# Optimization experiments

Hardware: AMD Instinct MI355X
Metric: run time of the kernel (lower is better)

The kernel has to match this reference:

```python
import jax, jax.numpy as jnp
import numpy as np

C_S = 128
C_T = 128
C_OUT = 128


def _proj(x, W, b):
    # 1x1x1 Conv3d == per-voxel linear over channel dim. x: [B, Cin, T, H, W]
    return jnp.einsum('oc,bcthw->bothw', W, x) + b[None, :, None, None, None]


def setup_inputs() -> dict:
    key = jax.random.key(0)
    ks = jax.random.split(key, 12)
    B, T, H, W = 4, 4, 32, 32
    spatial_features = jax.random.normal(ks[0], (B, T, C_S, H, W), dtype=jnp.float32)
    temporal_features = jax.random.normal(ks[1], (B, C_T, T, H, W), dtype=jnp.float32)
    def w(k, o, i):
        return jax.random.normal(k, (o, i), dtype=jnp.float32) * (i ** -0.5)
    return {
        'spatial_features': spatial_features,
        'temporal_features': temporal_features,
        'Wq': w(ks[2], C_OUT, C_S), 'bq': jnp.zeros((C_OUT,), jnp.float32),
        'Wk': w(ks[3], C_OUT, C_T), 'bk': jnp.zeros((C_OUT,), jnp.float32),
        'Wv': w(ks[4], C_OUT, C_T), 'bv': jnp.zeros((C_OUT,), jnp.float32),
        'Wo': w(ks[5], C_OUT, C_OUT), 'bo': jnp.zeros((C_OUT,), jnp.float32),
    }


def reference(spatial_features, temporal_features, Wq, bq, Wk, bk, Wv, bv, Wo, bo):
    B, T, C_s, H, W = spatial_features.shape
    N = T * H * W
    scale = C_OUT ** -0.5
    # permute(0,2,1,3,4): [B, T, C_s, H, W] -> [B, C_s, T, H, W]
    x_s = jnp.transpose(spatial_features, (0, 2, 1, 3, 4))
    q = _proj(x_s, Wq, bq)                 # [B, C_out, T, H, W]
    k = _proj(temporal_features, Wk, bk)   # [B, C_out, T, H, W]
    v = _proj(temporal_features, Wv, bv)   # [B, C_out, T, H, W]
    Q = q.reshape(B, C_OUT, N).transpose(0, 2, 1)  # [B, N, C]
    K = k.reshape(B, C_OUT, N)                     # [B, C, N]
    V = v.reshape(B, C_OUT, N).transpose(0, 2, 1)  # [B, N, C]
    attn = jax.nn.softmax(jnp.einsum('bnc,bcm->bnm', Q, K) * scale, axis=2)  # [B, N, N]
    out = jnp.einsum('bnm,bmc->bnc', attn, V)      # [B, N, C]
    out = out.transpose(0, 2, 1).reshape(B, C_OUT, T, H, W)
    return _proj(out, Wo, bo)
```

## Files before the change

kernel.cpp:

```cpp
#include <hip/hip_runtime.h>
#include <cstddef>

#define NDIM 4096
#define SCALE 0.08838834764831843f
#define SOFT_BIAS 8.0f

typedef _Float16 h8 __attribute__((ext_vector_type(8)));
typedef _Float16 h4 __attribute__((ext_vector_type(4)));
typedef _Float16 h2 __attribute__((ext_vector_type(2)));
typedef float    f4 __attribute__((ext_vector_type(4)));

__device__ __forceinline__ h8 cvt_w_frag(const float* wp) {
    const float4 u0 = *(const float4*)wp;
    const float4 u1 = *(const float4*)(wp + 4);
    h8 f;
    f[0]=(_Float16)u0.x; f[1]=(_Float16)u0.y; f[2]=(_Float16)u0.z; f[3]=(_Float16)u0.w;
    f[4]=(_Float16)u1.x; f[5]=(_Float16)u1.y; f[6]=(_Float16)u1.z; f[7]=(_Float16)u1.w;
    return f;
}

__global__ __launch_bounds__(256) void prep_w_kernel(
    const float* __restrict__ Wq, const float* __restrict__ Wk,
    const float* __restrict__ Wv, const float* __restrict__ Wo,
    _Float16* __restrict__ Whf)
{
    const int gid = blockIdx.x * 256 + threadIdx.x;
    const int mat = gid >> 11, rem = gid & 2047;
    const int ot = rem >> 8, ks = (rem >> 6) & 3, l = rem & 63;
    const float* src = mat == 0 ? Wq : mat == 1 ? Wk : mat == 2 ? Wv : Wo;
    const h8 f = cvt_w_frag(src + (size_t)(16 * ot + (l & 15)) * 128 + 32 * ks + 8 * (l >> 4));
    *(h8*)(Whf + (size_t)gid * 8) = f;
}

__global__ __launch_bounds__(256, 3) void proj_qkv_kernel(
    const float* __restrict__ spatial, const float* __restrict__ temporal,
    const _Float16* __restrict__ Whf,
    const float* __restrict__ bq, const float* __restrict__ bk,
    const float* __restrict__ bv,
    _Float16* __restrict__ Qh, _Float16* __restrict__ Kh, _Float16* __restrict__ Vt)
{
    __shared__ __align__(16) _Float16 Xl[32 * 136];
    const int tid = threadIdx.x;
    const int n0  = blockIdx.x * 32;
    const int b   = blockIdx.y;
    const int p   = blockIdx.z;
    const float* __restrict__ bias = (p == 0) ? bq : (p == 1) ? bk : bv;

    {
        const float* src; size_t rs;
        if (p == 0) { const int t = n0 >> 10, hw0 = n0 & 1023;
            src = spatial + (((size_t)(b * 4 + t) * 128) << 10) + hw0; rs = 1024; }
        else { src = temporal + ((size_t)(b * 128) << 12) + n0; rs = 4096; }
        #pragma unroll
        for (int i = 0; i < 2; ++i) {
            const int ii = tid + 256 * i;
            const int c2 = ii >> 3, j = ii & 7;
            const float4 v0 = *(const float4*)(src + (size_t)(2 * c2) * rs + 4 * j);
            const float4 v1 = *(const float4*)(src + (size_t)(2 * c2 + 1) * rs + 4 * j);
            const float a0[4] = {v0.x, v0.y, v0.z, v0.w};
            const float a1[4] = {v1.x, v1.y, v1.z, v1.w};
            #pragma unroll
            for (int u = 0; u < 4; ++u) {
                h2 pk; pk[0] = (_Float16)a0[u]; pk[1] = (_Float16)a1[u];
                *(h2*)&Xl[(4 * j + u) * 136 + 2 * c2] = pk;
            }
        }
    }
    __syncthreads();

    const int w = tid >> 6, lane = tid & 63, n16 = tid & 15, q4 = (tid >> 4) & 3;

    h8 wf[2][4];
    #pragma unroll
    for (int otl = 0; otl < 2; ++otl)
        #pragma unroll
        for (int ks = 0; ks < 4; ++ks)
            wf[otl][ks] = *(const h8*)(Whf + ((size_t)(((p * 8 + 2 * w + otl) * 4 + ks)) << 9)
                                           + lane * 8);
    h8 xf[2][4];
    #pragma unroll
    for (int ns = 0; ns < 2; ++ns)
        #pragma unroll
        for (int ks = 0; ks < 4; ++ks)
            xf[ns][ks] = *(const h8*)&Xl[(16 * ns + n16) * 136 + 32 * ks + 8 * q4];

    if (p < 2) {
        f4 acc[2][2];
        #pragma unroll
        for (int i = 0; i < 2; ++i) { acc[i][0] = (f4)0.0f; acc[i][1] = (f4)0.0f; }
        #pragma unroll
        for (int otl = 0; otl < 2; ++otl)
            #pragma unroll
            for (int ns = 0; ns < 2; ++ns)
                #pragma unroll
                for (int ks = 0; ks < 4; ++ks)
                    acc[otl][ns] = __builtin_amdgcn_mfma_f32_16x16x32_f16(
                        wf[otl][ks], xf[ns][ks], acc[otl][ns], 0, 0, 0);
        _Float16* __restrict__ dst = (p == 0) ? Qh : Kh;
        #pragma unroll
        for (int otl = 0; otl < 2; ++otl) {
            const float4 bb = *(const float4*)&bias[16 * (2 * w + otl) + 4 * q4];
            #pragma unroll
            for (int ns = 0; ns < 2; ++ns) {
                h4 r;
                r[0]=(_Float16)(acc[otl][ns][0]+bb.x); r[1]=(_Float16)(acc[otl][ns][1]+bb.y);
                r[2]=(_Float16)(acc[otl][ns][2]+bb.z); r[3]=(_Float16)(acc[otl][ns][3]+bb.w);
                *(h4*)(dst + ((size_t)b * NDIM + n0 + 16 * ns + n16) * 128
                           + 16 * (2 * w + otl) + 4 * q4) = r;
            }
        }
    } else {
        f4 acc[2][2];
        #pragma unroll
        for (int i = 0; i < 2; ++i) { acc[i][0] = (f4)0.0f; acc[i][1] = (f4)0.0f; }
        #pragma unroll
        for (int ns = 0; ns < 2; ++ns)
            #pragma unroll
            for (int otl = 0; otl < 2; ++otl)
                #pragma unroll
                for (int ks = 0; ks < 4; ++ks)
                    acc[ns][otl] = __builtin_amdgcn_mfma_f32_16x16x32_f16(
                        xf[ns][ks], wf[otl][ks], acc[ns][otl], 0, 0, 0);
        #pragma unroll
        for (int ns = 0; ns < 2; ++ns)
            #pragma unroll
            for (int otl = 0; otl < 2; ++otl) {
                const float bb = bias[16 * (2 * w + otl) + n16];
                h4 r;
                r[0]=(_Float16)(acc[ns][otl][0]+bb); r[1]=(_Float16)(acc[ns][otl][1]+bb);
                r[2]=(_Float16)(acc[ns][otl][2]+bb); r[3]=(_Float16)(acc[ns][otl][3]+bb);
                *(h4*)(Vt + ((size_t)(b * 128 + 16 * (2 * w + otl) + n16) << 12)
                          + n0 + 16 * ns + 4 * q4) = r;
            }
    }
}

__global__ __launch_bounds__(256, 2) void attn_kernel(
    const _Float16* __restrict__ Qh, const _Float16* __restrict__ Kh,
    const _Float16* __restrict__ Vt, _Float16* __restrict__ Opart,
    float* __restrict__ lpart)
{
    __shared__ __align__(16) _Float16 sh[29184];

    const int tid  = threadIdx.x;
    const int w    = tid >> 6, lane = tid & 63;
    const int g    = w >> 1,  p    = w & 1;
    const int n16  = lane & 15, q4 = lane >> 4;
    const int b    = blockIdx.z, hf = blockIdx.y;
    const int n0   = blockIdx.x * 128;
    const int mb   = hf * 1024;

    h8 qf[4][4];
    {
        const _Float16* Qb = Qh + ((size_t)b * NDIM + n0 + 64 * g + n16) * 128;
        #pragma unroll
        for (int qs = 0; qs < 4; ++qs)
            #pragma unroll
            for (int ks = 0; ks < 4; ++ks)
                qf[qs][ks] = *(const h8*)(Qb + (size_t)(16 * qs) * 128 + 32 * ks + 8 * q4);
    }

    const int km  = tid >> 4, kc8 = (tid & 15) * 8;
    const int vc  = tid >> 2, vm8 = (tid & 3) * 8;
    const _Float16* kp = Kh + ((size_t)b * NDIM + mb + km) * 128 + kc8;
    const _Float16* vp = Vt + (((size_t)(b * 128 + vc)) << 12) + mb + vm8;

    int4 kreg0 = *(const int4*)kp;
    int4 kreg1 = *(const int4*)(kp + (size_t)16 * 128);
    int4 vreg0 = *(const int4*)vp;
    int4 vreg1 = *(const int4*)(vp + ((size_t)64 << 12));
    *(int4*)&sh[km * 136 + kc8]        = kreg0;
    *(int4*)&sh[(16 + km) * 136 + kc8] = kreg1;
    kp += 32 * 128;
    kreg0 = *(const int4*)kp;
    kreg1 = *(const int4*)(kp + (size_t)16 * 128);

    f4 oacc[4][4];
    #pragma unroll
    for (int i = 0; i < 4; ++i)
        #pragma unroll
        for (int j = 0; j < 4; ++j) oacc[i][j] = (f4)0.0f;
    float lsum[4] = {0.0f, 0.0f, 0.0f, 0.0f};

    for (int it = 0; it < 32; ++it) {
        __syncthreads();
        const int cur = it & 1, prv = cur ^ 1;
        _Float16* __restrict__ KB = sh + cur * 4352;
        _Float16* __restrict__ KO = sh + prv * 4352;
        _Float16* __restrict__ VB = sh + 8704  + cur * 5120;
        const _Float16* __restrict__ VP = sh + 8704 + prv * 5120;
        _Float16* __restrict__ Pg = sh + 18944 + cur * 5120 + g * 2560;
        const _Float16* __restrict__ Pp = sh + 18944 + prv * 5120 + g * 2560;

        if (it > 0) {
            h8 pf[4], vf[4];
            #pragma unroll
            for (int qs = 0; qs < 4; ++qs)
                pf[qs] = *(const h8*)&Pp[(16 * qs + n16) * 40 + 8 * q4];
            #pragma unroll
            for (int ct = 0; ct < 4; ++ct)
                vf[ct] = *(const h8*)&VP[(64 * p + 16 * ct + n16) * 40 + 8 * q4];
            #pragma unroll
            for (int qs = 0; qs < 4; ++qs)
                #pragma unroll
                for (int ct = 0; ct < 4; ++ct)
                    oacc[qs][ct] = __builtin_amdgcn_mfma_f32_16x16x32_f16(
                        pf[qs], vf[ct], oacc[qs][ct], 0, 0, 0);
        }

        {
            f4 sacc[4];
            #pragma unroll
            for (int qs = 0; qs < 4; ++qs) sacc[qs] = (f4)0.0f;
            #pragma unroll
            for (int ks = 0; ks < 4; ++ks) {
                const h8 kf = *(const h8*)&KB[(16 * p + n16) * 136 + 32 * ks + 8 * q4];
                #pragma unroll
                for (int qs = 0; qs < 4; ++qs)
                    sacc[qs] = __builtin_amdgcn_mfma_f32_16x16x32_f16(kf, qf[qs][ks], sacc[qs], 0, 0, 0);
            }
            #pragma unroll
            for (int qs = 0; qs < 4; ++qs) {
                h4 pk;
                #pragma unroll
                for (int r = 0; r < 4; ++r) {
                    const float e = __expf(fmaf(sacc[qs][r], SCALE, -SOFT_BIAS));
                    lsum[qs] += e;
                    pk[r] = (_Float16)e;
                }
                *(h4*)&Pg[(16 * qs + n16) * 40 + 16 * p + 4 * q4] = pk;
            }
        }

        *(int4*)&VB[vc * 40 + vm8]        = vreg0;
        *(int4*)&VB[(64 + vc) * 40 + vm8] = vreg1;
        if (it < 31) {
            *(int4*)&KO[km * 136 + kc8]        = kreg0;
            *(int4*)&KO[(16 + km) * 136 + kc8] = kreg1;
            vp += 32;
            vreg0 = *(const int4*)vp;
            vreg1 = *(const int4*)(vp + ((size_t)64 << 12));
        }
        if (it < 30) {
            kp += 32 * 128;
            kreg0 = *(const int4*)kp;
            kreg1 = *(const int4*)(kp + (size_t)16 * 128);
        }
    }

    __syncthreads();
    {
        const _Float16* __restrict__ Pp = sh + 18944 + 5120 + g * 2560;
        const _Float16* __restrict__ VP = sh + 8704  + 5120;
        h8 pf[4], vf[4];
        #pragma unroll
        for (int qs = 0; qs < 4; ++qs)
            pf[qs] = *(const h8*)&Pp[(16 * qs + n16) * 40 + 8 * q4];
        #pragma unroll
        for (int ct = 0; ct < 4; ++ct)
            vf[ct] = *(const h8*)&VP[(64 * p + 16 * ct + n16) * 40 + 8 * q4];
        #pragma unroll
        for (int qs = 0; qs < 4; ++qs)
            #pragma unroll
            for (int ct = 0; ct < 4; ++ct)
                oacc[qs][ct] = __builtin_amdgcn_mfma_f32_16x16x32_f16(
                    pf[qs], vf[ct], oacc[qs][ct], 0, 0, 0);
    }

    #pragma unroll
    for (int qs = 0; qs < 4; ++qs) {
        lsum[qs] += __shfl_xor(lsum[qs], 16, 64);
        lsum[qs] += __shfl_xor(lsum[qs], 32, 64);
    }
    if (q4 == 0) {
        float* lb = lpart + ((size_t)((hf * 2 + p) * 4 + b)) * NDIM + n0 + 64 * g;
        #pragma unroll
        for (int qs = 0; qs < 4; ++qs) lb[16 * qs + n16] = lsum[qs];
    }

    __syncthreads();
    #pragma unroll
    for (int qs = 0; qs < 4; ++qs)
        #pragma unroll
        for (int ct = 0; ct < 4; ++ct)
            #pragma unroll
            for (int r = 0; r < 4; ++r)
                sh[(64 * g + 16 * qs + 4 * q4 + r) * 136 + 64 * p + 16 * ct + n16] =
                    (_Float16)oacc[qs][ct][r];
    __syncthreads();
    const size_t ob = ((size_t)(hf * 4 + b) * NDIM + n0) * 128;
    #pragma unroll
    for (int i = 0; i < 8; ++i) {
        const int ii  = tid + 256 * i;
        const int row = ii >> 4, c8 = (ii & 15) * 8;
        *(int4*)(Opart + ob + (size_t)row * 128 + c8) = *(const int4*)&sh[row * 136 + c8];
    }
}

__global__ __launch_bounds__(256, 2) void proj_final_kernel(
    const _Float16* __restrict__ Opart, const float* __restrict__ lpart,
    const _Float16* __restrict__ Whf, const float* __restrict__ bo,
    float* __restrict__ out)
{
    __shared__ __align__(16) _Float16 Xl[32 * 136];
    __shared__ float lrow[32];
    __shared__ __align__(16) float Ofin[128 * 36];
    const int tid = threadIdx.x;
    const int n0  = blockIdx.x * 32;
    const int b   = blockIdx.y;

    if (tid < 32) {
        float l = 0.0f;
        #pragma unroll
        for (int h8i = 0; h8i < 8; ++h8i)
            l += lpart[((size_t)(h8i * 4 + b)) * NDIM + n0 + tid];
        lrow[tid] = 1.0f / l;
    }
    float vals[2][8];
    int rows[2], c8s[2];
    #pragma unroll
    for (int i = 0; i < 2; ++i) {
        const int ii = tid + 256 * i;
        rows[i] = ii >> 4; c8s[i] = (ii & 15) * 8;
        #pragma unroll
        for (int j = 0; j < 8; ++j) vals[i][j] = 0.0f;
        #pragma unroll
        for (int hf = 0; hf < 4; ++hf) {
            const h8 o = *(const h8*)(Opart + ((size_t)(hf * 4 + b) * NDIM + n0 + rows[i]) * 128
                                      + c8s[i]);
            #pragma unroll
            for (int j = 0; j < 8; ++j) vals[i][j] += (float)o[j];
        }
    }
    __syncthreads();
    #pragma unroll
    for (int i = 0; i < 2; ++i) {
        const float linv = lrow[rows[i]];
        h8 r;
        #pragma unroll
        for (int j = 0; j < 8; ++j) r[j] = (_Float16)(vals[i][j] * linv);
        *(h8*)&Xl[rows[i] * 136 + c8s[i]] = r;
    }
    __syncthreads();

    const int w = tid >> 6, lane = tid & 63, n16 = tid & 15, q4 = (tid >> 4) & 3;

    h8 wf[2][4];
    #pragma unroll
    for (int otl = 0; otl < 2; ++otl)
        #pragma unroll
        for (int ks = 0; ks < 4; ++ks)
            wf[otl][ks] = *(const h8*)(Whf + ((size_t)(((3 * 8 + 2 * w + otl) * 4 + ks)) << 9)
                                           + lane * 8);
    h8 xf[2][4];
    #pragma unroll
    for (int ns = 0; ns < 2; ++ns)
        #pragma unroll
        for (int ks = 0; ks < 4; ++ks)
            xf[ns][ks] = *(const h8*)&Xl[(16 * ns + n16) * 136 + 32 * ks + 8 * q4];

    f4 acc[2][2];
    #pragma unroll
    for (int i = 0; i < 2; ++i) { acc[i][0] = (f4)0.0f; acc[i][1] = (f4)0.0f; }
    #pragma unroll
    for (int otl = 0; otl < 2; ++otl)
        #pragma unroll
        for (int ns = 0; ns < 2; ++ns)
            #pragma unroll
            for (int ks = 0; ks < 4; ++ks)
                acc[otl][ns] = __builtin_amdgcn_mfma_f32_16x16x32_f16(
                    wf[otl][ks], xf[ns][ks], acc[otl][ns], 0, 0, 0);

    #pragma unroll
    for (int otl = 0; otl < 2; ++otl) {
        const float4 bb = *(const float4*)&bo[16 * (2 * w + otl) + 4 * q4];
        const float bias[4] = {bb.x, bb.y, bb.z, bb.w};
        #pragma unroll
        for (int ns = 0; ns < 2; ++ns)
            #pragma unroll
            for (int r = 0; r < 4; ++r)
                Ofin[(16 * (2 * w + otl) + 4 * q4 + r) * 36 + 16 * ns + n16] =
                    acc[otl][ns][r] + bias[r];
    }
    __syncthreads();
    #pragma unroll
    for (int i = 0; i < 4; ++i) {
        const int ii  = tid + 256 * i;
        const int row = ii >> 3, j = ii & 7;
        *(float4*)(out + (((size_t)(b * 128 + row)) << 12) + n0 + 4 * j) =
            *(const float4*)&Ofin[row * 36 + 4 * j];
    }
}

extern "C" void kernel_launch(void* const* d_in, const int* in_sizes, int n_in,
                              void* d_out, int out_size, void* d_ws, size_t ws_size,
                              hipStream_t stream)
{
    const float* spatial  = (const float*)d_in[0];
    const float* temporal = (const float*)d_in[1];
    const float* Wq = (const float*)d_in[2];
    const float* bq = (const float*)d_in[3];
    const float* Wk = (const float*)d_in[4];
    const float* bk = (const float*)d_in[5];
    const float* Wv = (const float*)d_in[6];
    const float* bv = (const float*)d_in[7];
    const float* Wo = (const float*)d_in[8];
    const float* bo = (const float*)d_in[9];

    char* ws = (char*)d_ws;
    _Float16* Qh    = (_Float16*)(ws);
    _Float16* Kh    = (_Float16*)(ws + (4u  << 20));
    _Float16* Vt    = (_Float16*)(ws + (8u  << 20));
    _Float16* Opart = (_Float16*)(ws + (12u << 20));
    float*    lpart = (float*)   (ws + (28u << 20));
    _Float16* Whf   = (_Float16*)(ws + (28u << 20) + (512u << 10));

    prep_w_kernel<<<32, 256, 0, stream>>>(Wq, Wk, Wv, Wo, Whf);
    proj_qkv_kernel<<<dim3(128, 4, 3), 256, 0, stream>>>(
        spatial, temporal, Whf, bq, bk, bv, Qh, Kh, Vt);
    attn_kernel<<<dim3(32, 4, 4), 256, 0, stream>>>(Qh, Kh, Vt, Opart, lpart);
    proj_final_kernel<<<dim3(128, 4), 256, 0, stream>>>(Opart, lpart, Whf, bo,
                                                        (float*)d_out);
}
```

Baseline: 138.1 us.

## Keep softmax probabilities in registers for PV MFMA and stage QKV stores via LDS

The attention loop no longer writes P to shared memory and consumes it one iteration later. Each wave now feeds its exp'd scores straight from registers into 16x16x16 MFMAs against its own 16-key slice of V across all 128 output channels. The two waves that share a query group split the key dimension, so their partial outputs are reduced through LDS before the Opart store, and the shared-memory footprint drops. The QKV projection now stages results in LDS for coalesced 16-byte global stores and raises the occupancy hint. In exchange the accumulator registers double, the reduction adds extra syncs, and the cross-iteration overlap of P·V with QK^T is lost.

```diff
diff --git a/kernel.cpp b/kernel.cpp
--- a/kernel.cpp
+++ b/kernel.cpp
@@ -32,14 +32,14 @@
     *(h8*)(Whf + (size_t)gid * 8) = f;
 }
 
-__global__ __launch_bounds__(256, 3) void proj_qkv_kernel(
+__global__ __launch_bounds__(256, 4) void proj_qkv_kernel(
     const float* __restrict__ spatial, const float* __restrict__ temporal,
     const _Float16* __restrict__ Whf,
     const float* __restrict__ bq, const float* __restrict__ bk,
     const float* __restrict__ bv,
     _Float16* __restrict__ Qh, _Float16* __restrict__ Kh, _Float16* __restrict__ Vt)
 {
-    __shared__ __align__(16) _Float16 Xl[32 * 136];
+    __shared__ __align__(16) _Float16 shb[4608];
     const int tid = threadIdx.x;
     const int n0  = blockIdx.x * 32;
     const int b   = blockIdx.y;
@@ -62,7 +62,7 @@
             #pragma unroll
             for (int u = 0; u < 4; ++u) {
                 h2 pk; pk[0] = (_Float16)a0[u]; pk[1] = (_Float16)a1[u];
-                *(h2*)&Xl[(4 * j + u) * 136 + 2 * c2] = pk;
+                *(h2*)&shb[(4 * j + u) * 136 + 2 * c2] = pk;
             }
         }
     }
@@ -82,7 +82,8 @@
     for (int ns = 0; ns < 2; ++ns)
         #pragma unroll
         for (int ks = 0; ks < 4; ++ks)
-            xf[ns][ks] = *(const h8*)&Xl[(16 * ns + n16) * 136 + 32 * ks + 8 * q4];
+            xf[ns][ks] = *(const h8*)&shb[(16 * ns + n16) * 136 + 32 * ks + 8 * q4];
+    __syncthreads();
 
     if (p < 2) {
         f4 acc[2][2];
@@ -96,18 +97,26 @@
                 for (int ks = 0; ks < 4; ++ks)
                     acc[otl][ns] = __builtin_amdgcn_mfma_f32_16x16x32_f16(
                         wf[otl][ks], xf[ns][ks], acc[otl][ns], 0, 0, 0);
-        _Float16* __restrict__ dst = (p == 0) ? Qh : Kh;
         #pragma unroll
         for (int otl = 0; otl < 2; ++otl) {
             const float4 bb = *(const float4*)&bias[16 * (2 * w + otl) + 4 * q4];
+            const float bias4[4] = {bb.x, bb.y, bb.z, bb.w};
             #pragma unroll
             for (int ns = 0; ns < 2; ++ns) {
                 h4 r;
-                r[0]=(_Float16)(acc[otl][ns][0]+bb.x); r[1]=(_Float16)(acc[otl][ns][1]+bb.y);
-                r[2]=(_Float16)(acc[otl][ns][2]+bb.z); r[3]=(_Float16)(acc[otl][ns][3]+bb.w);
-                *(h4*)(dst + ((size_t)b * NDIM + n0 + 16 * ns + n16) * 128
-                           + 16 * (2 * w + otl) + 4 * q4) = r;
+                #pragma unroll
+                for (int rr = 0; rr < 4; ++rr) r[rr] = (_Float16)(acc[otl][ns][rr] + bias4[rr]);
+                *(h4*)&shb[(16 * ns + n16) * 136 + 16 * (2 * w + otl) + 4 * q4] = r;
             }
+        }
+        __syncthreads();
+        _Float16* __restrict__ dst = (p == 0) ? Qh : Kh;
+        #pragma unroll
+        for (int i = 0; i < 2; ++i) {
+            const int ii = tid + 256 * i;
+            const int row = ii >> 4, c8 = (ii & 15) * 8;
+            *(int4*)(dst + ((size_t)b * NDIM + n0 + row) * 128 + c8) =
+                *(const int4*)&shb[row * 136 + c8];
         }
     } else {
         f4 acc[2][2];
@@ -127,11 +136,18 @@
             for (int otl = 0; otl < 2; ++otl) {
                 const float bb = bias[16 * (2 * w + otl) + n16];
                 h4 r;
-                r[0]=(_Float16)(acc[ns][otl][0]+bb); r[1]=(_Float16)(acc[ns][otl][1]+bb);
-                r[2]=(_Float16)(acc[ns][otl][2]+bb); r[3]=(_Float16)(acc[ns][otl][3]+bb);
-                *(h4*)(Vt + ((size_t)(b * 128 + 16 * (2 * w + otl) + n16) << 12)
-                          + n0 + 16 * ns + 4 * q4) = r;
+                #pragma unroll
+                for (int rr = 0; rr < 4; ++rr) r[rr] = (_Float16)(acc[ns][otl][rr] + bb);
+                *(h4*)&shb[(16 * (2 * w + otl) + n16) * 36 + 16 * ns + 4 * q4] = r;
             }
+        __syncthreads();
+        #pragma unroll
+        for (int i = 0; i < 2; ++i) {
+            const int ii = tid + 256 * i;
+            const int row = ii >> 2, n8 = (ii & 3) * 8;
+            *(int4*)(Vt + (((size_t)(b * 128 + row)) << 12) + n0 + n8) =
+                *(const int4*)&shb[row * 36 + n8];
+        }
     }
 }
 
@@ -140,7 +156,7 @@
     const _Float16* __restrict__ Vt, _Float16* __restrict__ Opart,
     float* __restrict__ lpart)
 {
-    __shared__ __align__(16) _Float16 sh[29184];
+    __shared__ __align__(16) _Float16 sh[18944];
 
     const int tid  = threadIdx.x;
     const int w    = tid >> 6, lane = tid & 63;
@@ -169,102 +185,75 @@
     int4 kreg1 = *(const int4*)(kp + (size_t)16 * 128);
     int4 vreg0 = *(const int4*)vp;
     int4 vreg1 = *(const int4*)(vp + ((size_t)64 << 12));
-    *(int4*)&sh[km * 136 + kc8]        = kreg0;
-    *(int4*)&sh[(16 + km) * 136 + kc8] = kreg1;
-    kp += 32 * 128;
+    *(int4*)&sh[km * 136 + kc8]               = kreg0;
+    *(int4*)&sh[(16 + km) * 136 + kc8]        = kreg1;
+    *(int4*)&sh[8704 + vc * 40 + vm8]         = vreg0;
+    *(int4*)&sh[8704 + (64 + vc) * 40 + vm8]  = vreg1;
+    kp += 32 * 128; vp += 32;
     kreg0 = *(const int4*)kp;
     kreg1 = *(const int4*)(kp + (size_t)16 * 128);
-
-    f4 oacc[4][4];
+    vreg0 = *(const int4*)vp;
+    vreg1 = *(const int4*)(vp + ((size_t)64 << 12));
+
+    f4 oacc[4][8];
     #pragma unroll
     for (int i = 0; i < 4; ++i)
         #pragma unroll
-        for (int j = 0; j < 4; ++j) oacc[i][j] = (f4)0.0f;
+        for (int j = 0; j < 8; ++j) oacc[i][j] = (f4)0.0f;
     float lsum[4] = {0.0f, 0.0f, 0.0f, 0.0f};
 
     for (int it = 0; it < 32; ++it) {
         __syncthreads();
-        const int cur = it & 1, prv = cur ^ 1;
-        _Float16* __restrict__ KB = sh + cur * 4352;
-        _Float16* __restrict__ KO = sh + prv * 4352;
-        _Float16* __restrict__ VB = sh + 8704  + cur * 5120;
-        const _Float16* __restrict__ VP = sh + 8704 + prv * 5120;
-        _Float16* __restrict__ Pg = sh + 18944 + cur * 5120 + g * 2560;
-        const _Float16* __restrict__ Pp = sh + 18944 + prv * 5120 + g * 2560;
-
-        if (it > 0) {
-            h8 pf[4], vf[4];
+        const int cur = it & 1, nxt = cur ^ 1;
+        const _Float16* __restrict__ KB = sh + cur * 4352;
+        const _Float16* __restrict__ VB = sh + 8704 + cur * 5120;
+
+        f4 sacc[4];
+        #pragma unroll
+        for (int qs = 0; qs < 4; ++qs) sacc[qs] = (f4)0.0f;
+        #pragma unroll
+        for (int ks = 0; ks < 4; ++ks) {
+            const h8 kf = *(const h8*)&KB[(16 * p + n16) * 136 + 32 * ks + 8 * q4];
             #pragma unroll
             for (int qs = 0; qs < 4; ++qs)
-                pf[qs] = *(const h8*)&Pp[(16 * qs + n16) * 40 + 8 * q4];
-            #pragma unroll
-            for (int ct = 0; ct < 4; ++ct)
-                vf[ct] = *(const h8*)&VP[(64 * p + 16 * ct + n16) * 40 + 8 * q4];
+                sacc[qs] = __builtin_amdgcn_mfma_f32_16x16x32_f16(kf, qf[qs][ks], sacc[qs], 0, 0, 0);
+        }
+
+        h4 pf[4];
+        #pragma unroll
+        for (int qs = 0; qs < 4; ++qs) {
+            #pragma unroll
+            for (int r = 0; r < 4; ++r) {
+                const float e = __expf(fmaf(sacc[qs][r], SCALE, -SOFT_BIAS));
+                lsum[qs] += e;
+                pf[qs][r] = (_Float16)e;
+            }
+        }
+
+        #pragma unroll
+        for (int ct = 0; ct < 8; ++ct) {
+            const h4 vf = *(const h4*)&VB[(16 * ct + n16) * 40 + 16 * p + 4 * q4];
             #pragma unroll
             for (int qs = 0; qs < 4; ++qs)
-                #pragma unroll
-                for (int ct = 0; ct < 4; ++ct)
-                    oacc[qs][ct] = __builtin_amdgcn_mfma_f32_16x16x32_f16(
-                        pf[qs], vf[ct], oacc[qs][ct], 0, 0, 0);
-        }
-
-        {
-            f4 sacc[4];
-            #pragma unroll
-            for (int qs = 0; qs < 4; ++qs) sacc[qs] = (f4)0.0f;
-            #pragma unroll
-            for (int ks = 0; ks < 4; ++ks) {
-                const h8 kf = *(const h8*)&KB[(16 * p + n16) * 136 + 32 * ks + 8 * q4];
-                #pragma unroll
-                for (int qs = 0; qs < 4; ++qs)
-                    sacc[qs] = __builtin_amdgcn_mfma_f32_16x16x32_f16(kf, qf[qs][ks], sacc[qs], 0, 0, 0);
-            }
-            #pragma unroll
-            for (int qs = 0; qs < 4; ++qs) {
-                h4 pk;
-                #pragma unroll
-                for (int r = 0; r < 4; ++r) {
-                    const float e = __expf(fmaf(sacc[qs][r], SCALE, -SOFT_BIAS));
-                    lsum[qs] += e;
-                    pk[r] = (_Float16)e;
-                }
-                *(h4*)&Pg[(16 * qs + n16) * 40 + 16 * p + 4 * q4] = pk;
-            }
-        }
-
-        *(int4*)&VB[vc * 40 + vm8]        = vreg0;
-        *(int4*)&VB[(64 + vc) * 40 + vm8] = vreg1;
+                oacc[qs][ct] = __builtin_amdgcn_mfma_f32_16x16x16f16(
+                    pf[qs], vf, oacc[qs][ct], 0, 0, 0);
+        }
+
         if (it < 31) {
-            *(int4*)&KO[km * 136 + kc8]        = kreg0;
-            *(int4*)&KO[(16 + km) * 136 + kc8] = kreg1;
-            vp += 32;
+            _Float16* __restrict__ KN = sh + nxt * 4352;
+            _Float16* __restrict__ VN = sh + 8704 + nxt * 5120;
+            *(int4*)&KN[km * 136 + kc8]        = kreg0;
+            *(int4*)&KN[(16 + km) * 136 + kc8] = kreg1;
+            *(int4*)&VN[vc * 40 + vm8]         = vreg0;
+            *(int4*)&VN[(64 + vc) * 40 + vm8]  = vreg1;
+        }
+        if (it < 30) {
+            kp += 32 * 128; vp += 32;
+            kreg0 = *(const int4*)kp;
+            kreg1 = *(const int4*)(kp + (size_t)16 * 128);
             vreg0 = *(const int4*)vp;
             vreg1 = *(const int4*)(vp + ((size_t)64 << 12));
         }
-        if (it < 30) {
-            kp += 32 * 128;
-            kreg0 = *(const int4*)kp;
-            kreg1 = *(const int4*)(kp + (size_t)16 * 128);
-        }
-    }
-
-    __syncthreads();
-    {
-        const _Float16* __restrict__ Pp = sh + 18944 + 5120 + g * 2560;
-        const _Float16* __restrict__ VP = sh + 8704  + 5120;
-        h8 pf[4], vf[4];
-        #pragma unroll
-        for (int qs = 0; qs < 4; ++qs)
-            pf[qs] = *(const h8*)&Pp[(16 * qs + n16) * 40 + 8 * q4];
-        #pragma unroll
-        for (int ct = 0; ct < 4; ++ct)
-            vf[ct] = *(const h8*)&VP[(64 * p + 16 * ct + n16) * 40 + 8 * q4];
-        #pragma unroll
-        for (int qs = 0; qs < 4; ++qs)
-            #pragma unroll
-            for (int ct = 0; ct < 4; ++ct)
-                oacc[qs][ct] = __builtin_amdgcn_mfma_f32_16x16x32_f16(
-                    pf[qs], vf[ct], oacc[qs][ct], 0, 0, 0);
     }
 
     #pragma unroll
@@ -278,22 +267,39 @@
         for (int qs = 0; qs < 4; ++qs) lb[16 * qs + n16] = lsum[qs];
     }
 
-    __syncthreads();
-    #pragma unroll
-    for (int qs = 0; qs < 4; ++qs)
-        #pragma unroll
-        for (int ct = 0; ct < 4; ++ct)
-            #pragma unroll
-            for (int r = 0; r < 4; ++r)
-                sh[(64 * g + 16 * qs + 4 * q4 + r) * 136 + 64 * p + 16 * ct + n16] =
-                    (_Float16)oacc[qs][ct][r];
-    __syncthreads();
-    const size_t ob = ((size_t)(hf * 4 + b) * NDIM + n0) * 128;
-    #pragma unroll
-    for (int i = 0; i < 8; ++i) {
-        const int ii  = tid + 256 * i;
-        const int row = ii >> 4, c8 = (ii & 15) * 8;
-        *(int4*)(Opart + ob + (size_t)row * 128 + c8) = *(const int4*)&sh[row * 136 + c8];
+    float* __restrict__ shf = (float*)sh;
+    for (int g2 = 0; g2 < 2; ++g2) {
+        __syncthreads();
+        if (g == g2 && p == 0) {
+            #pragma unroll
+            for (int qs = 0; qs < 4; ++qs)
+                #pragma unroll
+                for (int ct = 0; ct < 8; ++ct)
+                    #pragma unroll
+                    for (int r = 0; r < 4; ++r)
+                        shf[(16 * qs + 4 * q4 + r) * 132 + 16 * ct + n16] = oacc[qs][ct][r];
+        }
+        __syncthreads();
+        if (g == g2 && p == 1) {
+            #pragma unroll
+            for (int qs = 0; qs < 4; ++qs)
+                #pragma unroll
+                for (int ct = 0; ct < 8; ++ct)
+                    #pragma unroll
+                    for (int r = 0; r < 4; ++r)
+                        shf[(16 * qs + 4 * q4 + r) * 132 + 16 * ct + n16] += oacc[qs][ct][r];
+        }
+        __syncthreads();
+        const size_t ob = ((size_t)(hf * 4 + b) * NDIM + n0 + 64 * g2) * 128;
+        #pragma unroll
+        for (int i = 0; i < 4; ++i) {
+            const int ii  = tid + 256 * i;
+            const int row = ii >> 4, c8 = (ii & 15) * 8;
+            h8 r;
+            #pragma unroll
+            for (int j = 0; j < 8; ++j) r[j] = (_Float16)shf[row * 132 + c8 + j];
+            *(h8*)(Opart + ob + (size_t)row * 128 + c8) = r;
+        }
     }
 }
 
```

After: 144.4 us. 1.05x slower.
